# Kernel tuning notes

Hardware: AMD Instinct MI355X
Metric: run time of the kernel (lower is better)

Reference implementation:

```python
import jax, jax.numpy as jnp
import numpy as np

EPS = 1e-06  # params.eps
B, N, D, L = 8, 512, 768, 16


def focal_loss(y_true, y_pred, gamma=2.0, alpha=0.5):
    # tf.where(y==1, -a*(1-p)^g*log(p), -(1-a)*p^g*log(1-p))
    pos = -alpha * (1.0 - y_pred) ** gamma * jnp.log(y_pred)
    neg = -(1.0 - alpha) * y_pred ** gamma * jnp.log(1.0 - y_pred)
    return jnp.where(y_true == 1, pos, neg)


def setup_inputs() -> dict:
    key = jax.random.key(0)
    ks = jax.random.split(key, 10)
    x = jax.random.normal(ks[0], (B, N, D), jnp.float32)
    start = jax.random.randint(ks[1], (B, L, N), 0, 2).astype(jnp.float32)
    end = jax.random.randint(ks[2], (B, L, N), 0, 2).astype(jnp.float32)
    span = jax.random.randint(ks[3], (B, L, N, N), 0, 2).astype(jnp.int32)
    val = jax.random.randint(ks[4], (B, L, N, N), 0, 2).astype(jnp.int32)
    seqlen = jax.random.randint(ks[5], (B,), N // 2, N + 1).astype(jnp.int32)
    # Dense kernels, TruncatedNormal(stddev=0.02) ~ 0.02*randn is close enough
    W_se = 0.02 * jax.random.normal(ks[6], (D, 2 * L), jnp.float32)
    b_se = jnp.zeros((2 * L,), jnp.float32)
    W_span = 0.02 * jax.random.normal(ks[7], (2 * D, L), jnp.float32)
    b_span = jnp.zeros((L,), jnp.float32)
    return dict(x=x, start=start, end=end, span=span, val=val, seqlen=seqlen,
                W_se=W_se, b_se=b_se, W_span=W_span, b_span=b_span)


def reference(x, start, end, span, val, seqlen, W_se, b_se, W_span, b_span):
    b, n, d = x.shape
    l = b_span.shape[0]
    # ---- start/end branch ----
    se = jax.nn.sigmoid(x @ W_se + b_se)              # [B,N,2L]
    se = jnp.transpose(se, (0, 2, 1))                 # [B,2L,N]
    startend = jnp.concatenate([start, end], axis=1)  # [B,2L,N]
    se_loss = focal_loss(startend, se)                # [B,2L,N]
    seqmask = (jnp.arange(n)[None, :] < seqlen[:, None]).astype(jnp.float32)  # [B,N]
    mask2 = jnp.broadcast_to(seqmask[:, None, :], (b, 2 * l, n))
    startend_loss = jnp.sum(se_loss * mask2) / jnp.sum(mask2)
    # ---- span branch ----
    # Dense(concat(x_i, x_j)) == x_i @ W_a + x_j @ W_b + bias  (biaffine decomposition),
    # avoiding the O(N^2 * 2D) tiled concat tensor.
    a = x @ W_span[:d]                                # [B,N,L] start-side
    bb = x @ W_span[d:]                               # [B,N,L] end-side
    logits = a[:, :, None, :] + bb[:, None, :, :] + b_span  # [B,N,N,L]
    span_output = jnp.transpose(jax.nn.sigmoid(logits), (0, 3, 1, 2))  # [B,L,N,N]
    span_predict = (span_output > 0.5).astype(jnp.int32)
    valf = val.astype(jnp.float32)
    valsum = jnp.sum(valf) + EPS
    tp = jnp.sum(((span == 1) & (span_predict == 1)).astype(jnp.float32))
    tn = jnp.sum(((span == 1) & (span_predict != 1)).astype(jnp.float32))
    fp = jnp.sum(((span == 0) & (val == 1) & (span_predict == 1)).astype(jnp.float32))
    span_loss = jnp.sum(focal_loss(span, span_output) * valf) / valsum
    return span_predict, tp, tn, fp, startend_loss, span_loss
```

## Files before the change

kernel.cpp:

```cpp
#include <hip/hip_runtime.h>

#define Bsz 8
#define Nn  512
#define Dd  768
#define Ll  16

#define SPAN_BLOCKS 2048
#define PREP_BLOCKS (Bsz * (Nn / 8))


__global__ __launch_bounds__(256) void k_prep(
    const float* __restrict__ x, const float* __restrict__ start,
    const float* __restrict__ end, const int* __restrict__ seqlen,
    const float* __restrict__ W_se, const float* __restrict__ b_se,
    const float* __restrict__ W_span, const float* __restrict__ b_span,
    float* __restrict__ At, float* __restrict__ Bt, float* __restrict__ se_part)
{
    __shared__ float xs[8 * Dd];
    __shared__ float part[256 * 8];
    __shared__ float s_se;

    const int tid = threadIdx.x;
    const int blk = blockIdx.x;
    const int b   = blk >> 6;
    const int n0  = (blk & 63) * 8;

    if (tid == 0) s_se = 0.0f;

    const float4* xsrc = (const float4*)(x + (size_t)(b * Nn + n0) * Dd);
    float4* xd = (float4*)xs;
    for (int i = tid; i < 8 * Dd / 4; i += 256) xd[i] = xsrc[i];
    __syncthreads();

    const int c = tid & 63;
    const int q = tid >> 6;

    float a8[8];
#pragma unroll
    for (int r = 0; r < 8; ++r) a8[r] = 0.0f;

    const float* w;
    int stride;
    if (c < 32)       { w = W_se + c;                    stride = 32; }
    else if (c < 48)  { w = W_span + (c - 32);           stride = 16; }
    else              { w = W_span + Dd * 16 + (c - 48); stride = 16; }

    const int k0 = q * 192;
#pragma unroll 4
    for (int k = k0; k < k0 + 192; ++k) {
        const float wv = w[(size_t)k * stride];
#pragma unroll
        for (int r = 0; r < 8; ++r) a8[r] += xs[r * Dd + k] * wv;
    }
#pragma unroll
    for (int r = 0; r < 8; ++r) part[tid * 8 + r] = a8[r];
    __syncthreads();

    if (tid < 64) {
        float z[8];
#pragma unroll
        for (int r = 0; r < 8; ++r)
            z[r] = part[c * 8 + r] + part[(c + 64) * 8 + r] +
                   part[(c + 128) * 8 + r] + part[(c + 192) * 8 + r];

        if (c < 32) {
            const int sl = seqlen[b];
            float lsum = 0.0f;
            const float bse = b_se[c];
#pragma unroll
            for (int r = 0; r < 8; ++r) {
                const int n = n0 + r;
                const float zz = z[r] + bse;
                const float p = 1.0f / (1.0f + __expf(-zz));
                const float y = (c < 16) ? start[(b * Ll + c) * Nn + n]
                                         : end[(b * Ll + (c - 16)) * Nn + n];
                const float fl = (y == 1.0f)
                    ? (-0.5f * (1.0f - p) * (1.0f - p) * __logf(p))
                    : (-0.5f * p * p * __logf(1.0f - p));
                if (n < sl) lsum += fl;
            }
            atomicAdd(&s_se, lsum);
        } else if (c < 48) {
            const int l = c - 32;
            const float bsp = b_span[l];
#pragma unroll
            for (int r = 0; r < 8; ++r)
                At[(b * Ll + l) * Nn + n0 + r] = z[r] + bsp;
        } else {
            const int l = c - 48;
#pragma unroll
            for (int r = 0; r < 8; ++r)
                Bt[(b * Ll + l) * Nn + n0 + r] = z[r];
        }
    }
    __syncthreads();
    if (tid == 0) se_part[blk] = s_se;
}

__global__ __launch_bounds__(256) void k_span(
    const float* __restrict__ At, const float* __restrict__ Bt,
    const int* __restrict__ span, const int* __restrict__ val,
    float* __restrict__ out, float* __restrict__ pb)
{
    const int tid = threadIdx.x;
    const int base0 = blockIdx.x * (256 * 16) + tid;

    const int4*  s4 = (const int4*)span;
    const int4*  v4 = (const int4*)val;
    float4*      o4 = (float4*)out;

    int tpc = 0, tnc = 0, fpc = 0, vc = 0;
    float ls = 0.0f;

#define DO_ELEM(aa, btj, spv, vvv, pout)                                      \
    {                                                                         \
        const float z = (aa) + (btj);                                         \
        const int pred = (z > 0.0f) ? 1 : 0;                                  \
        (pout) = pred ? 1.0f : 0.0f;                                          \
        tpc += ((spv) == 1) & pred;                                           \
        tnc += ((spv) == 1) & (pred ^ 1);                                     \
        fpc += ((spv) == 0) & ((vvv) == 1) & pred;                            \
        vc  += (vvv);                                                         \
        const float t = ((spv) == 1) ? z : -z;                                \
        const float u = __expf(-t);                                           \
        const float d = 1.0f + u;                                             \
        const float m = u * __builtin_amdgcn_rcpf(d);                         \
        const float fl = 0.5f * m * m * __logf(d);                            \
        ls += (vvv) ? fl : 0.0f;                                              \
    }

    int4 csp = s4[base0], cvv = v4[base0];

#pragma unroll
    for (int st = 0; st < 16; ++st) {
        const int vid = base0 + st * 256;

        const int ri = vid >> 7;
        const float  av = At[ri];
        const float4 bt = *(const float4*)(Bt + ((ri >> 9) << 9) + ((vid & 127) << 2));
        __builtin_amdgcn_sched_barrier(0);

        int4 nsp, nvv;
        if (st < 15) { nsp = s4[vid + 256]; nvv = v4[vid + 256]; }
        __builtin_amdgcn_sched_barrier(0);

        float4 po;
        DO_ELEM(av, bt.x, csp.x, cvv.x, po.x)
        DO_ELEM(av, bt.y, csp.y, cvv.y, po.y)
        DO_ELEM(av, bt.z, csp.z, cvv.z, po.z)
        DO_ELEM(av, bt.w, csp.w, cvv.w, po.w)
        o4[vid] = po;

        if (st < 15) { csp = nsp; cvv = nvv; }
    }
#undef DO_ELEM

    for (int off = 32; off; off >>= 1) {
        tpc += __shfl_down(tpc, off);
        tnc += __shfl_down(tnc, off);
        fpc += __shfl_down(fpc, off);
        vc  += __shfl_down(vc,  off);
        ls  += __shfl_down(ls,  off);
    }

    __shared__ int   si[4][4];
    __shared__ float sf[4];
    const int wave = tid >> 6, lane = tid & 63;
    if (lane == 0) {
        si[wave][0] = tpc; si[wave][1] = tnc; si[wave][2] = fpc; si[wave][3] = vc;
        sf[wave] = ls;
    }
    __syncthreads();
    if (tid == 0) {
        int t0 = 0, t1 = 0, t2 = 0, t3 = 0;
        float f = 0.0f;
        for (int w = 0; w < 4; ++w) {
            t0 += si[w][0]; t1 += si[w][1]; t2 += si[w][2]; t3 += si[w][3];
            f += sf[w];
        }
        float* dst = pb + blockIdx.x * 8;
        dst[0] = (float)t0;
        dst[1] = (float)t1;
        dst[2] = (float)t2;
        dst[3] = (float)t3;
        dst[4] = f;
    }
}

__global__ __launch_bounds__(256) void k_fin(
    const float* __restrict__ pb, const float* __restrict__ se_part,
    const int* __restrict__ seqlen, float* __restrict__ out5)
{
    const int tid = threadIdx.x;
    long long t0 = 0, t1 = 0, t2 = 0, t3 = 0;
    float f = 0.0f, se = 0.0f;

    for (int i = tid; i < SPAN_BLOCKS; i += 256) {
        const float4 p0 = *(const float4*)(pb + i * 8);
        const float  p4 = pb[i * 8 + 4];
        t0 += (long long)p0.x; t1 += (long long)p0.y;
        t2 += (long long)p0.z; t3 += (long long)p0.w;
        f  += p4;
    }
    for (int i = tid; i < PREP_BLOCKS; i += 256) se += se_part[i];

    for (int off = 32; off; off >>= 1) {
        t0 += __shfl_down(t0, off);
        t1 += __shfl_down(t1, off);
        t2 += __shfl_down(t2, off);
        t3 += __shfl_down(t3, off);
        f  += __shfl_down(f,  off);
        se += __shfl_down(se, off);
    }

    __shared__ long long sl[4][4];
    __shared__ float sfl[4][2];
    const int wave = tid >> 6, lane = tid & 63;
    if (lane == 0) {
        sl[wave][0] = t0; sl[wave][1] = t1; sl[wave][2] = t2; sl[wave][3] = t3;
        sfl[wave][0] = f; sfl[wave][1] = se;
    }
    __syncthreads();
    if (tid == 0) {
        long long a0 = 0, a1 = 0, a2 = 0, a3 = 0;
        float af = 0.0f, ase = 0.0f;
        for (int w = 0; w < 4; ++w) {
            a0 += sl[w][0]; a1 += sl[w][1]; a2 += sl[w][2]; a3 += sl[w][3];
            af += sfl[w][0]; ase += sfl[w][1];
        }
        int ssum = 0;
        for (int i = 0; i < Bsz; ++i) ssum += seqlen[i];
        out5[0] = (float)a0;
        out5[1] = (float)a1;
        out5[2] = (float)a2;
        out5[3] = ase / (2.0f * Ll * (float)ssum);
        out5[4] = af / ((float)a3 + 1e-6f);
    }
}

extern "C" void kernel_launch(void* const* d_in, const int* in_sizes, int n_in,
                              void* d_out, int out_size, void* d_ws, size_t ws_size,
                              hipStream_t stream) {
    const float* x      = (const float*)d_in[0];
    const float* start  = (const float*)d_in[1];
    const float* end    = (const float*)d_in[2];
    const int*   span   = (const int*)d_in[3];
    const int*   val    = (const int*)d_in[4];
    const int*   seqlen = (const int*)d_in[5];
    const float* W_se   = (const float*)d_in[6];
    const float* b_se   = (const float*)d_in[7];
    const float* W_span = (const float*)d_in[8];
    const float* b_span = (const float*)d_in[9];

    float* out = (float*)d_out;

    const size_t n_at = (size_t)Bsz * Ll * Nn;
    float* At      = (float*)d_ws;
    float* Bt      = At + n_at;
    float* se_part = Bt + n_at;
    float* pb      = se_part + PREP_BLOCKS;

    k_prep<<<PREP_BLOCKS, 256, 0, stream>>>(x, start, end, seqlen,
                                            W_se, b_se, W_span, b_span,
                                            At, Bt, se_part);

    const long long total_elems = (long long)Bsz * Ll * Nn * Nn;
    k_span<<<SPAN_BLOCKS, 256, 0, stream>>>(At, Bt, span, val, out, pb);

    k_fin<<<1, 256, 0, stream>>>(pb, se_part, seqlen, out + total_elems);
}
```

Baseline: 373.9 us.

## Hand-pipeline span kernel loads with inline asm and explicit vmcnt waits

Replaces the compiler-scheduled loop in the span kernel with inline-assembly global loads and stores on a three-deep rotating register buffer, using explicit s_waitcnt vmcnt counts to keep several span/val loads in flight while computing earlier stages. The Bt vector is loaded once per thread and the At scalar via immediate offsets. The goal is to hide memory latency in a bandwidth-bound streaming kernel. The hand-counted waitcnt values are fragile, and any miscount would produce races or stalls.

```diff
diff --git a/kernel.cpp b/kernel.cpp
--- a/kernel.cpp
+++ b/kernel.cpp
@@ -7,6 +7,9 @@
 
 #define SPAN_BLOCKS 2048
 #define PREP_BLOCKS (Bsz * (Nn / 8))
+
+typedef int   i32x4 __attribute__((ext_vector_type(4)));
+typedef float f32x4 __attribute__((ext_vector_type(4)));
 
 
 __global__ __launch_bounds__(256) void k_prep(
@@ -105,14 +108,45 @@
     const int tid = threadIdx.x;
     const int base0 = blockIdx.x * (256 * 16) + tid;
 
-    const int4*  s4 = (const int4*)span;
-    const int4*  v4 = (const int4*)val;
-    float4*      o4 = (float4*)out;
-
     int tpc = 0, tnc = 0, fpc = 0, vc = 0;
     float ls = 0.0f;
 
-#define DO_ELEM(aa, btj, spv, vvv, pout)                                      \
+    unsigned voff_pf = (unsigned)base0 * 16u;
+    unsigned voff_st = voff_pf;
+    const int ri0 = base0 >> 7;
+    const unsigned voff_av = (unsigned)ri0 << 2;
+    const unsigned voff_bt = (((unsigned)base0 >> 16) << 11)
+                           | (((unsigned)base0 & 127u) << 4);
+
+    i32x4 sp0, sp1, sp2, vv0, vv1, vv2;
+    float av0, av1;
+    f32x4 bt, po0, po1, po2;
+
+#define LD_BT() \
+    asm volatile("global_load_dwordx4 %0, %1, %2" \
+                 : "=v"(bt) : "v"(voff_bt), "s"(Bt) : "memory");
+
+#define LD_SPVV(SPX, VVX) \
+    asm volatile("global_load_dwordx4 %0, %2, %3\n\t" \
+                 "global_load_dwordx4 %1, %2, %4" \
+                 : "=v"(SPX), "=v"(VVX) \
+                 : "v"(voff_pf), "s"(span), "s"(val) : "memory"); \
+    voff_pf += 4096u;
+
+#define LD_AV(AVX, OFFSTR) \
+    asm volatile("global_load_dword %0, %1, %2 offset:" OFFSTR \
+                 : "=v"(AVX) : "v"(voff_av), "s"(At) : "memory");
+
+#define ST_OUT(POX) \
+    asm volatile("global_store_dwordx4 %0, %1, %2" \
+                 :: "v"(voff_st), "v"(POX), "s"(out) : "memory"); \
+    voff_st += 4096u;
+
+#define WAITK(KSTR) \
+    asm volatile("s_waitcnt vmcnt(" KSTR ")" ::: "memory"); \
+    __builtin_amdgcn_sched_barrier(0);
+
+#define COMP1(aa, btj, spv, vvv, pout)                                        \
     {                                                                         \
         const float z = (aa) + (btj);                                         \
         const int pred = (z > 0.0f) ? 1 : 0;                                  \
@@ -129,31 +163,64 @@
         ls += (vvv) ? fl : 0.0f;                                              \
     }
 
-    int4 csp = s4[base0], cvv = v4[base0];
-
-#pragma unroll
-    for (int st = 0; st < 16; ++st) {
-        const int vid = base0 + st * 256;
-
-        const int ri = vid >> 7;
-        const float  av = At[ri];
-        const float4 bt = *(const float4*)(Bt + ((ri >> 9) << 9) + ((vid & 127) << 2));
-        __builtin_amdgcn_sched_barrier(0);
-
-        int4 nsp, nvv;
-        if (st < 15) { nsp = s4[vid + 256]; nvv = v4[vid + 256]; }
-        __builtin_amdgcn_sched_barrier(0);
-
-        float4 po;
-        DO_ELEM(av, bt.x, csp.x, cvv.x, po.x)
-        DO_ELEM(av, bt.y, csp.y, cvv.y, po.y)
-        DO_ELEM(av, bt.z, csp.z, cvv.z, po.z)
-        DO_ELEM(av, bt.w, csp.w, cvv.w, po.w)
-        o4[vid] = po;
-
-        if (st < 15) { csp = nsp; cvv = nvv; }
-    }
-#undef DO_ELEM
+#define COMPUTE(SPX, VVX, AVX, POX)            \
+    COMP1(AVX, bt.x, SPX.x, VVX.x, POX.x)      \
+    COMP1(AVX, bt.y, SPX.y, VVX.y, POX.y)      \
+    COMP1(AVX, bt.z, SPX.z, VVX.z, POX.z)      \
+    COMP1(AVX, bt.w, SPX.w, VVX.w, POX.w)
+
+    LD_BT()
+    LD_SPVV(sp0, vv0)
+    LD_SPVV(sp1, vv1)
+    LD_AV(av0, "0")
+    LD_AV(av1, "8")
+    LD_SPVV(sp2, vv2)
+
+#define STAGE_MID(KSTR, SPX, VVX, AVX, POX, AOFF)  \
+    WAITK(KSTR)                                    \
+    COMPUTE(SPX, VVX, AVX, POX)                    \
+    LD_AV(AVX, AOFF)                               \
+    LD_SPVV(SPX, VVX)                              \
+    ST_OUT(POX)
+
+    STAGE_MID("3", sp0, vv0, av0, po0, "16")
+    STAGE_MID("6", sp1, vv1, av1, po1, "24")
+    STAGE_MID("7", sp2, vv2, av0, po2, "32")
+    STAGE_MID("7", sp0, vv0, av1, po0, "40")
+    STAGE_MID("7", sp1, vv1, av0, po1, "48")
+    STAGE_MID("7", sp2, vv2, av1, po2, "56")
+    STAGE_MID("7", sp0, vv0, av0, po0, "64")
+    STAGE_MID("7", sp1, vv1, av1, po1, "72")
+    STAGE_MID("7", sp2, vv2, av0, po2, "80")
+    STAGE_MID("7", sp0, vv0, av1, po0, "88")
+    STAGE_MID("7", sp1, vv1, av0, po1, "96")
+    STAGE_MID("7", sp2, vv2, av1, po2, "104")
+    STAGE_MID("7", sp0, vv0, av0, po0, "112")
+
+    WAITK("7")
+    COMPUTE(sp1, vv1, av1, po1)
+    LD_AV(av1, "120")
+    ST_OUT(po1)
+
+    WAITK("5")
+    COMPUTE(sp2, vv2, av0, po2)
+    ST_OUT(po2)
+
+    WAITK("2")
+    COMPUTE(sp0, vv0, av1, po0)
+    ST_OUT(po0)
+
+    asm volatile("s_waitcnt vmcnt(0)" ::: "memory");
+    __builtin_amdgcn_sched_barrier(0);
+
+#undef STAGE_MID
+#undef COMPUTE
+#undef COMP1
+#undef WAITK
+#undef ST_OUT
+#undef LD_AV
+#undef LD_SPVV
+#undef LD_BT
 
     for (int off = 32; off; off >>= 1) {
         tpc += __shfl_down(tpc, off);
@@ -264,8 +331,7 @@
                                             W_se, b_se, W_span, b_span,
                                             At, Bt, se_part);
 
-    const long long total_elems = (long long)Bsz * Ll * Nn * Nn;
     k_span<<<SPAN_BLOCKS, 256, 0, stream>>>(At, Bt, span, val, out, pb);
 
-    k_fin<<<1, 256, 0, stream>>>(pb, se_part, seqlen, out + total_elems);
+    k_fin<<<1, 256, 0, stream>>>(pb, se_part, seqlen, out + (long long)Bsz * Ll * Nn * Nn);
 }
```

After: 371.7 us. Within noise of the previous version (-0.6%).

## Split span kernel into separate stats and prediction-write kernels

Applied to the files above, without the earlier changes.

Splits the fused span kernel into two kernels. One reads span/val and reduces the counts and focal loss. The other only writes the thresholded predictions. Each thread now hoists its Bt float4 load out of the loop, since the column stays fixed across iterations, and the manual prefetch and sched barriers are removed. This separates the read-heavy and write-heavy streams so each can reach bandwidth on its own, at the cost of an extra launch and re-reading At/Bt.

```diff
diff --git a/kernel.cpp b/kernel.cpp
--- a/kernel.cpp
+++ b/kernel.cpp
@@ -97,26 +97,27 @@
     if (tid == 0) se_part[blk] = s_se;
 }
 
-__global__ __launch_bounds__(256) void k_span(
+__global__ __launch_bounds__(256) void k_stats(
     const float* __restrict__ At, const float* __restrict__ Bt,
     const int* __restrict__ span, const int* __restrict__ val,
-    float* __restrict__ out, float* __restrict__ pb)
+    float* __restrict__ pb)
 {
     const int tid = threadIdx.x;
     const int base0 = blockIdx.x * (256 * 16) + tid;
 
-    const int4*  s4 = (const int4*)span;
-    const int4*  v4 = (const int4*)val;
-    float4*      o4 = (float4*)out;
+    const int4* s4 = (const int4*)span;
+    const int4* v4 = (const int4*)val;
+
+    const float4 bt = *(const float4*)(Bt + ((base0 >> 16) << 9) + ((base0 & 127) << 2));
+    const int ri0 = base0 >> 7;
 
     int tpc = 0, tnc = 0, fpc = 0, vc = 0;
     float ls = 0.0f;
 
-#define DO_ELEM(aa, btj, spv, vvv, pout)                                      \
+#define DO_ELEM(aa, btj, spv, vvv)                                            \
     {                                                                         \
         const float z = (aa) + (btj);                                         \
         const int pred = (z > 0.0f) ? 1 : 0;                                  \
-        (pout) = pred ? 1.0f : 0.0f;                                          \
         tpc += ((spv) == 1) & pred;                                           \
         tnc += ((spv) == 1) & (pred ^ 1);                                     \
         fpc += ((spv) == 0) & ((vvv) == 1) & pred;                            \
@@ -129,29 +130,16 @@
         ls += (vvv) ? fl : 0.0f;                                              \
     }
 
-    int4 csp = s4[base0], cvv = v4[base0];
-
 #pragma unroll
     for (int st = 0; st < 16; ++st) {
         const int vid = base0 + st * 256;
-
-        const int ri = vid >> 7;
-        const float  av = At[ri];
-        const float4 bt = *(const float4*)(Bt + ((ri >> 9) << 9) + ((vid & 127) << 2));
-        __builtin_amdgcn_sched_barrier(0);
-
-        int4 nsp, nvv;
-        if (st < 15) { nsp = s4[vid + 256]; nvv = v4[vid + 256]; }
-        __builtin_amdgcn_sched_barrier(0);
-
-        float4 po;
-        DO_ELEM(av, bt.x, csp.x, cvv.x, po.x)
-        DO_ELEM(av, bt.y, csp.y, cvv.y, po.y)
-        DO_ELEM(av, bt.z, csp.z, cvv.z, po.z)
-        DO_ELEM(av, bt.w, csp.w, cvv.w, po.w)
-        o4[vid] = po;
-
-        if (st < 15) { csp = nsp; cvv = nvv; }
+        const int4 sp = s4[vid];
+        const int4 vv = v4[vid];
+        const float av = At[ri0 + 2 * st];
+        DO_ELEM(av, bt.x, sp.x, vv.x)
+        DO_ELEM(av, bt.y, sp.y, vv.y)
+        DO_ELEM(av, bt.z, sp.z, vv.z)
+        DO_ELEM(av, bt.w, sp.w, vv.w)
     }
 #undef DO_ELEM
 
@@ -184,6 +172,30 @@
         dst[2] = (float)t2;
         dst[3] = (float)t3;
         dst[4] = f;
+    }
+}
+
+__global__ __launch_bounds__(256) void k_pred(
+    const float* __restrict__ At, const float* __restrict__ Bt,
+    float* __restrict__ out)
+{
+    const int tid = threadIdx.x;
+    const int base0 = blockIdx.x * (256 * 16) + tid;
+    float4* o4 = (float4*)out;
+
+    const float4 bt = *(const float4*)(Bt + ((base0 >> 16) << 9) + ((base0 & 127) << 2));
+    const int ri0 = base0 >> 7;
+
+#pragma unroll
+    for (int st = 0; st < 16; ++st) {
+        const int vid = base0 + st * 256;
+        const float av = At[ri0 + 2 * st];
+        float4 po;
+        po.x = (av + bt.x > 0.0f) ? 1.0f : 0.0f;
+        po.y = (av + bt.y > 0.0f) ? 1.0f : 0.0f;
+        po.z = (av + bt.z > 0.0f) ? 1.0f : 0.0f;
+        po.w = (av + bt.w > 0.0f) ? 1.0f : 0.0f;
+        o4[vid] = po;
     }
 }
 
@@ -264,8 +276,8 @@
                                             W_se, b_se, W_span, b_span,
                                             At, Bt, se_part);
 
-    const long long total_elems = (long long)Bsz * Ll * Nn * Nn;
-    k_span<<<SPAN_BLOCKS, 256, 0, stream>>>(At, Bt, span, val, out, pb);
-
-    k_fin<<<1, 256, 0, stream>>>(pb, se_part, seqlen, out + total_elems);
-}
+    k_stats<<<SPAN_BLOCKS, 256, 0, stream>>>(At, Bt, span, val, pb);
+    k_pred <<<SPAN_BLOCKS, 256, 0, stream>>>(At, Bt, out);
+
+    k_fin<<<1, 256, 0, stream>>>(pb, se_part, seqlen, out + (long long)Bsz * Ll * Nn * Nn);
+}
```

Result: slower. 381.9 us (+2.1%).
